# Optimization experiments

Hardware: AMD Instinct MI355X
Metric: run time of the kernel (lower is better)

The kernel has to match this reference:

```python
import jax, jax.numpy as jnp
import numpy as np

N_NODES = 50000
N_GRAPHS = 64


def _gcn_layer(x, w, b, src, dst, dinv):
    # GCNConv: out = D^{-1/2} (A+I) D^{-1/2} (x W) + b; self-loops already in src/dst
    xw = x @ w                                  # [N, out]
    norm = (dinv[src] * dinv[dst])[:, None]     # [E+N, 1]
    msgs = xw[src] * norm                       # gather + scale
    out = jax.ops.segment_sum(msgs, dst, num_segments=N_NODES)
    return out + b


def setup_inputs() -> dict:
    key = jax.random.key(0)
    ks = jax.random.split(key, 12)
    E = 800000
    F_IN, H = 128, 256
    x = jax.random.normal(ks[0], (N_NODES, F_IN), dtype=jnp.float32)
    edge_attr = jax.random.normal(ks[1], (E, 4), dtype=jnp.float32)
    edge_index = jax.random.randint(ks[2], (2, E), 0, N_NODES, dtype=jnp.int64)
    batch = jnp.sort(jax.random.randint(ks[3], (N_NODES,), 0, N_GRAPHS, dtype=jnp.int64))
    def glorot(k, fi, fo):
        s = jnp.sqrt(6.0 / (fi + fo))
        return jax.random.uniform(k, (fi, fo), minval=-s, maxval=s, dtype=jnp.float32)
    return {
        "x": x, "edge_attr": edge_attr, "edge_index": edge_index, "batch": batch,
        "w1": glorot(ks[4], F_IN, H), "b1": jnp.zeros((H,), jnp.float32),
        "w2": glorot(ks[5], H, H), "b2": jnp.zeros((H,), jnp.float32),
        "w3": glorot(ks[6], H, H), "b3": jnp.zeros((H,), jnp.float32),
        "lin1_w": glorot(ks[7], H, H // 2), "lin1_b": jnp.zeros((H // 2,), jnp.float32),
        "lin2_w": glorot(ks[8], H // 2, 3), "lin2_b": jnp.zeros((3,), jnp.float32),
    }


def reference(x, edge_attr, edge_index, batch, w1, b1, w2, b2, w3, b3,
              lin1_w, lin1_b, lin2_w, lin2_b):
    # add self-loops once; shared by all three conv layers
    loop = jnp.arange(N_NODES, dtype=edge_index.dtype)
    src = jnp.concatenate([edge_index[0], loop])
    dst = jnp.concatenate([edge_index[1], loop])
    deg = jax.ops.segment_sum(jnp.ones_like(dst, dtype=x.dtype), dst, num_segments=N_NODES)
    dinv = jnp.where(deg > 0, jax.lax.rsqrt(deg), 0.0)

    h = jax.nn.relu(_gcn_layer(x, w1, b1, src, dst, dinv))
    h = jax.nn.relu(_gcn_layer(h, w2, b2, src, dst, dinv))
    h = _gcn_layer(h, w3, b3, src, dst, dinv)

    # global mean pool over graphs
    sums = jax.ops.segment_sum(h, batch, num_segments=N_GRAPHS)
    cnts = jax.ops.segment_sum(jnp.ones((h.shape[0],), h.dtype), batch, num_segments=N_GRAPHS)
    pooled = sums / jnp.maximum(cnts, 1.0)[:, None]

    # eval mode: dropout is identity
    out = pooled @ lin1_w + lin1_b
    out = out @ lin2_w + lin2_b
    return out
```

## Files before the change

### kernel.cpp

```cpp
#include <hip/hip_runtime.h>
#include <cstdint>

constexpr int NG = 64;
constexpr int H  = 256;

typedef __bf16 bf16x8 __attribute__((ext_vector_type(8)));
typedef float  f32x4  __attribute__((ext_vector_type(4)));

__device__ __forceinline__ uint32_t pk_bf16(float a, float b) {
    uint32_t ua = __builtin_bit_cast(uint32_t, a);
    uint32_t ub = __builtin_bit_cast(uint32_t, b);
    ua += 0x7fffu + ((ua >> 16) & 1u);
    ub += 0x7fffu + ((ub >> 16) & 1u);
    return (ua >> 16) | (ub & 0xffff0000u);
}
__device__ __forceinline__ ushort bf16r(float x) {
    uint32_t u = __builtin_bit_cast(uint32_t, x);
    u += 0x7fffu + ((u >> 16) & 1u);
    return (ushort)(u >> 16);
}
__device__ __forceinline__ float bf2f(ushort h) {
    return __builtin_bit_cast(float, ((uint32_t)h) << 16);
}
__device__ __forceinline__ void bf2acc(uint32_t u, float& a0, float& a1) {
    a0 += __builtin_bit_cast(float, u << 16);
    a1 += __builtin_bit_cast(float, u & 0xffff0000u);
}

__global__ void hist_kernel(const int* __restrict__ dst, int* __restrict__ cnt, int E) {
    int e = blockIdx.x * blockDim.x + threadIdx.x;
    if (e < E) atomicAdd(&cnt[dst[e]], 1);
}

__global__ __launch_bounds__(256) void scanA(const int* __restrict__ cnt, int* __restrict__ bsum,
                                             float* __restrict__ dinv, int n) {
    __shared__ int sh[256];
    int t = threadIdx.x, i = blockIdx.x * 256 + t;
    int v = (i < n) ? cnt[i] : 0;
    if (i < n) dinv[i] = rsqrtf((float)(v + 1));
    sh[t] = v;
    __syncthreads();
    for (int off = 128; off > 0; off >>= 1) {
        if (t < off) sh[t] += sh[t + off];
        __syncthreads();
    }
    if (t == 0) bsum[blockIdx.x] = sh[0];
}

__global__ __launch_bounds__(256) void scanB(const int* __restrict__ bsum, int* __restrict__ boff,
                                             int* __restrict__ total_out, int nb) {
    __shared__ int sh[256];
    int t = threadIdx.x;
    int v = (t < nb) ? bsum[t] : 0;
    sh[t] = v;
    __syncthreads();
    for (int off = 1; off < 256; off <<= 1) {
        int a = (t >= off) ? sh[t - off] : 0;
        __syncthreads();
        sh[t] += a;
        __syncthreads();
    }
    if (t < nb) boff[t] = sh[t] - v;
    if (t == nb - 1) *total_out = sh[t];
}

__global__ __launch_bounds__(256) void scanC(const int* __restrict__ cnt, const int* __restrict__ boff,
                                             int* __restrict__ row_ptr, int* __restrict__ fill, int n) {
    __shared__ int sh[256];
    int t = threadIdx.x, i = blockIdx.x * 256 + t;
    int v = (i < n) ? cnt[i] : 0;
    sh[t] = v;
    __syncthreads();
    for (int off = 1; off < 256; off <<= 1) {
        int a = (t >= off) ? sh[t - off] : 0;
        __syncthreads();
        sh[t] += a;
        __syncthreads();
    }
    if (i < n) {
        int excl = boff[blockIdx.x] + sh[t] - v;
        row_ptr[i] = excl;
        fill[i] = excl;
    }
}

__global__ void sp_kernel(const int* __restrict__ src, const int* __restrict__ dst,
                          int* __restrict__ fill, int* __restrict__ ssrc, int E,
                          const float* __restrict__ x, const float* __restrict__ dinv,
                          ushort* __restrict__ y, int np4 ) {
    int i = blockIdx.x * blockDim.x + threadIdx.x;
    if (i < E) {
        int pos = atomicAdd(&fill[dst[i]], 1);
        ssrc[pos] = src[i];
    }
    if (i < np4) {
        int f = i * 4;
        float dv = dinv[f >> 7];
        float4 v = *reinterpret_cast<const float4*>(x + f);
        uint2 o;
        o.x = pk_bf16(v.x * dv, v.y * dv);
        o.y = pk_bf16(v.z * dv, v.w * dv);
        *reinterpret_cast<uint2*>(y + f) = o;
    }
}

__global__ void wconv_kernel(const float* __restrict__ w1, ushort* __restrict__ h1, ushort* __restrict__ l1,
                             const float* __restrict__ w2, ushort* __restrict__ h2, ushort* __restrict__ l2) {
    int idx = blockIdx.x * 256 + threadIdx.x;
    const float* w; ushort *hi, *lo; int K;
    if (idx < 128 * 256) { w = w1; hi = h1; lo = l1; K = 128; }
    else { idx -= 128 * 256; if (idx >= 256 * 256) return; w = w2; hi = h2; lo = l2; K = 256; }
    int k = idx / 256, n = idx & 255;
    float v = w[idx];
    ushort h = bf16r(v);
    float r = v - bf2f(h);
    hi[n * K + k] = h;
    lo[n * K + k] = bf16r(r);
}

template<int VEC>
__global__ __launch_bounds__(256) void agg_kernel(const ushort* __restrict__ y,
                                                  const float* __restrict__ dinv,
                                                  const int* __restrict__ row_ptr,
                                                  const int* __restrict__ ssrc,
                                                  ushort* __restrict__ zout, int n) {
    constexpr int W = VEC * 64;
    int wave = threadIdx.x >> 6;
    int lane = threadIdx.x & 63;
    int node = blockIdx.x * 4 + wave;
    if (node >= n) return;
    float acc[VEC] = {};

    auto ld4 = [&](int s) -> uint2 {
        return *reinterpret_cast<const uint2*>(y + (size_t)s * W + lane * VEC);
    };
    auto ld2 = [&](int s) -> uint32_t {
        return *reinterpret_cast<const uint32_t*>(y + (size_t)s * W + lane * VEC);
    };

    if constexpr (VEC == 4) {
        uint2 v = ld4(node);
        bf2acc(v.x, acc[0], acc[1]); bf2acc(v.y, acc[2], acc[3]);
    } else {
        bf2acc(ld2(node), acc[0], acc[1]);
    }

    int beg = row_ptr[node], end = row_ptr[node + 1];
    int e = beg;
    for (; e + 8 <= end; e += 8) {
        int s[8];
        #pragma unroll
        for (int q = 0; q < 8; ++q) s[q] = ssrc[e + q];
        if constexpr (VEC == 4) {
            uint2 v[8];
            #pragma unroll
            for (int q = 0; q < 8; ++q) v[q] = ld4(s[q]);
            #pragma unroll
            for (int q = 0; q < 8; ++q) {
                bf2acc(v[q].x, acc[0], acc[1]); bf2acc(v[q].y, acc[2], acc[3]);
            }
        } else {
            uint32_t v[8];
            #pragma unroll
            for (int q = 0; q < 8; ++q) v[q] = ld2(s[q]);
            #pragma unroll
            for (int q = 0; q < 8; ++q) bf2acc(v[q], acc[0], acc[1]);
        }
    }
    for (; e + 4 <= end; e += 4) {
        int s[4];
        #pragma unroll
        for (int q = 0; q < 4; ++q) s[q] = ssrc[e + q];
        if constexpr (VEC == 4) {
            uint2 v[4];
            #pragma unroll
            for (int q = 0; q < 4; ++q) v[q] = ld4(s[q]);
            #pragma unroll
            for (int q = 0; q < 4; ++q) {
                bf2acc(v[q].x, acc[0], acc[1]); bf2acc(v[q].y, acc[2], acc[3]);
            }
        } else {
            uint32_t v[4];
            #pragma unroll
            for (int q = 0; q < 4; ++q) v[q] = ld2(s[q]);
            #pragma unroll
            for (int q = 0; q < 4; ++q) bf2acc(v[q], acc[0], acc[1]);
        }
    }
    for (; e < end; ++e) {
        if constexpr (VEC == 4) {
            uint2 v = ld4(ssrc[e]);
            bf2acc(v.x, acc[0], acc[1]); bf2acc(v.y, acc[2], acc[3]);
        } else {
            bf2acc(ld2(ssrc[e]), acc[0], acc[1]);
        }
    }

    float dv = dinv[node];
    ushort* zp = zout + (size_t)node * W + lane * VEC;
    if constexpr (VEC == 4) {
        uint2 o;
        o.x = pk_bf16(dv * acc[0], dv * acc[1]);
        o.y = pk_bf16(dv * acc[2], dv * acc[3]);
        *reinterpret_cast<uint2*>(zp) = o;
    } else {
        *reinterpret_cast<uint32_t*>(zp) = pk_bf16(dv * acc[0], dv * acc[1]);
    }
}

template<bool RELU>
__global__ __launch_bounds__(256) void mfma_gemm(const ushort* __restrict__ A,
                                                 const ushort* __restrict__ Bhi,
                                                 const ushort* __restrict__ Blo,
                                                 const float* __restrict__ bias,
                                                 const float* __restrict__ dinv,
                                                 ushort* __restrict__ C, int M, int K) {
    constexpr int BM = 128, BN = 64, BK = 64;
    constexpr int LDK = BK + 8;
    __shared__ ushort As[BM][LDK];
    __shared__ ushort Bh[BN][LDK];
    __shared__ ushort Bl[BN][LDK];

    const int tid = threadIdx.x;
    const int w = tid >> 6;
    const int l = tid & 63;
    const int lr = l & 15;
    const int lk = (l >> 4) * 8;
    const int bm = blockIdx.x * BM;
    const int bn = blockIdx.y * BN;

    f32x4 acc[8];
    #pragma unroll
    for (int i = 0; i < 8; ++i) acc[i] = (f32x4){0.f, 0.f, 0.f, 0.f};

    for (int k0 = 0; k0 < K; k0 += BK) {
        #pragma unroll
        for (int p = 0; p < 4; ++p) {
            int g = tid + p * 256;
            int r = g >> 3;
            int c = (g & 7) << 3;
            int grow = bm + r;
            uint4 va = make_uint4(0u, 0u, 0u, 0u);
            if (grow < M) va = *reinterpret_cast<const uint4*>(A + (size_t)grow * K + k0 + c);
            *reinterpret_cast<uint4*>(&As[r][c]) = va;
        }
        #pragma unroll
        for (int p = 0; p < 2; ++p) {
            int g = tid + p * 256;
            int r = g >> 3;
            int c = (g & 7) << 3;
            *reinterpret_cast<uint4*>(&Bh[r][c]) =
                *reinterpret_cast<const uint4*>(Bhi + (size_t)(bn + r) * K + k0 + c);
            *reinterpret_cast<uint4*>(&Bl[r][c]) =
                *reinterpret_cast<const uint4*>(Blo + (size_t)(bn + r) * K + k0 + c);
        }
        __syncthreads();
        #pragma unroll
        for (int kk = 0; kk < BK; kk += 32) {
            bf16x8 bh = *reinterpret_cast<const bf16x8*>(&Bh[w * 16 + lr][kk + lk]);
            bf16x8 bl = *reinterpret_cast<const bf16x8*>(&Bl[w * 16 + lr][kk + lk]);
            #pragma unroll
            for (int r16 = 0; r16 < 8; ++r16) {
                bf16x8 a = *reinterpret_cast<const bf16x8*>(&As[r16 * 16 + lr][kk + lk]);
                acc[r16] = __builtin_amdgcn_mfma_f32_16x16x32_bf16(a, bh, acc[r16], 0, 0, 0);
                acc[r16] = __builtin_amdgcn_mfma_f32_16x16x32_bf16(a, bl, acc[r16], 0, 0, 0);
            }
        }
        __syncthreads();
    }

    int col = bn + w * 16 + lr;
    float bv = bias[col];
    #pragma unroll
    for (int r16 = 0; r16 < 8; ++r16) {
        #pragma unroll
        for (int j = 0; j < 4; ++j) {
            int row = bm + r16 * 16 + (l >> 4) * 4 + j;
            if (row < M) {
                float v = acc[r16][j] + bv;
                if (RELU) v = fmaxf(v, 0.f);
                v *= dinv[row];
                C[(size_t)row * H + col] = bf16r(v);
            }
        }
    }
}

__global__ __launch_bounds__(256) void pool_kernel(const ushort* __restrict__ z,
                                                   const int* __restrict__ batch,
                                                   float* __restrict__ sums,
                                                   int* __restrict__ gcnt, int n) {
    constexpr int NCH = 128;
    int t = threadIdx.x;
    int base = blockIdx.x * NCH;
    if (base >= n) return;
    int endn = min(base + NCH, n);
    int cur = batch[base];
    float local = 0.f;
    int cl = 0;
    for (int i = base; i < endn; ++i) {
        int g = batch[i];
        if (g != cur) {
            atomicAdd(&sums[cur * H + t], local);
            if (t == 0) atomicAdd(&gcnt[cur], cl);
            local = 0.f; cl = 0; cur = g;
        }
        local += bf2f(z[(size_t)i * H + t]);
        cl++;
    }
    atomicAdd(&sums[cur * H + t], local);
    if (t == 0) atomicAdd(&gcnt[cur], cl);
}

__global__ __launch_bounds__(256) void head_kernel(const float* __restrict__ sums,
                                                   const int* __restrict__ gcnt,
                                                   const float* __restrict__ w3, const float* __restrict__ b3,
                                                   const float* __restrict__ l1w, const float* __restrict__ l1b,
                                                   const float* __restrict__ l2w, const float* __restrict__ l2b,
                                                   float* __restrict__ out) {
    __shared__ float pooled[H];
    __shared__ float t3[H];
    __shared__ float mid[H / 2];
    int g = blockIdx.x, t = threadIdx.x;
    float c = (float)max(gcnt[g], 1);
    pooled[t] = sums[g * H + t] / c;
    __syncthreads();
    float a = b3[t];
    for (int k = 0; k < H; ++k) a += pooled[k] * w3[k * H + t];
    t3[t] = a;
    __syncthreads();
    if (t < H / 2) {
        float m = l1b[t];
        for (int k = 0; k < H; ++k) m += t3[k] * l1w[k * (H / 2) + t];
        mid[t] = m;
    }
    __syncthreads();
    if (t < 3) {
        float o = l2b[t];
        for (int k = 0; k < H / 2; ++k) o += mid[k] * l2w[k * 3 + t];
        out[g * 3 + t] = o;
    }
}

extern "C" void kernel_launch(void* const* d_in, const int* in_sizes, int n_in,
                              void* d_out, int out_size, void* d_ws, size_t ws_size,
                              hipStream_t stream) {
    const float* x   = (const float*)d_in[0];
    const int*   ei  = (const int*)d_in[2];
    const int*   bat = (const int*)d_in[3];
    const float* w1  = (const float*)d_in[4];
    const float* b1  = (const float*)d_in[5];
    const float* w2  = (const float*)d_in[6];
    const float* b2  = (const float*)d_in[7];
    const float* w3  = (const float*)d_in[8];
    const float* b3  = (const float*)d_in[9];
    const float* l1w = (const float*)d_in[10];
    const float* l1b = (const float*)d_in[11];
    const float* l2w = (const float*)d_in[12];
    const float* l2b = (const float*)d_in[13];
    float* out = (float*)d_out;

    const int N = in_sizes[0] / 128;
    const int E = in_sizes[2] / 2;
    const int NB = (N + 255) / 256;

    char* ws = (char*)d_ws;
    size_t off = 0;
    auto alloc = [&](size_t bytes) {
        void* p = ws + off;
        off = (off + bytes + 255) & ~(size_t)255;
        return p;
    };
    ushort* yb     = (ushort*)alloc((size_t)N * H * 2);
    ushort* z16    = (ushort*)alloc((size_t)N * H * 2);
    int*    cnt    = (int*)alloc((size_t)N * 4);
    float*  dinv   = (float*)alloc((size_t)N * 4);
    int*    row_ptr= (int*)alloc((size_t)(N + 1) * 4);
    int*    fill   = (int*)alloc((size_t)N * 4);
    int*    ssrc   = (int*)alloc((size_t)E * 4);
    int*    bsum   = (int*)alloc(256 * 4);
    int*    boff   = (int*)alloc(256 * 4);
    ushort* wt1h   = (ushort*)alloc((size_t)128 * 256 * 2);
    ushort* wt1l   = (ushort*)alloc((size_t)128 * 256 * 2);
    ushort* wt2h   = (ushort*)alloc((size_t)256 * 256 * 2);
    ushort* wt2l   = (ushort*)alloc((size_t)256 * 256 * 2);
    float*  sums   = (float*)alloc((size_t)NG * H * 4);
    int*    gcnt   = (int*)alloc((size_t)NG * 4);

    hipMemsetAsync(cnt, 0, (size_t)N * 4, stream);
    hipMemsetAsync(sums, 0, (size_t)NG * H * 4, stream);
    hipMemsetAsync(gcnt, 0, (size_t)NG * 4, stream);

    hist_kernel<<<(E + 255) / 256, 256, 0, stream>>>(ei + E, cnt, E);
    scanA<<<NB, 256, 0, stream>>>(cnt, bsum, dinv, N);
    scanB<<<1, 256, 0, stream>>>(bsum, boff, row_ptr + N, NB);
    scanC<<<NB, 256, 0, stream>>>(cnt, boff, row_ptr, fill, N);
    wconv_kernel<<<(128 * 256 + 256 * 256) / 256, 256, 0, stream>>>(w1, wt1h, wt1l, w2, wt2h, wt2l);
    sp_kernel<<<(N * 32 + 255) / 256, 256, 0, stream>>>(ei, ei + E, fill, ssrc, E,
                                                        x, dinv, yb, N * 32);

    agg_kernel<2><<<(N + 3) / 4, 256, 0, stream>>>(yb, dinv, row_ptr, ssrc, z16, N);
    mfma_gemm<true><<<dim3((N + 127) / 128, 4), 256, 0, stream>>>(z16, wt1h, wt1l, b1, dinv, yb, N, 128);

    agg_kernel<4><<<(N + 3) / 4, 256, 0, stream>>>(yb, dinv, row_ptr, ssrc, z16, N);
    mfma_gemm<true><<<dim3((N + 127) / 128, 4), 256, 0, stream>>>(z16, wt2h, wt2l, b2, dinv, yb, N, 256);

    agg_kernel<4><<<(N + 3) / 4, 256, 0, stream>>>(yb, dinv, row_ptr, ssrc, z16, N);

    pool_kernel<<<(N + 127) / 128, 256, 0, stream>>>(z16, bat, sums, gcnt, N);
    head_kernel<<<NG, 256, 0, stream>>>(sums, gcnt, w3, b3, l1w, l1b, l2w, l2b, out);
}
```

Baseline: 470.0 us.

## Store features in 32-column chunk planes and split aggregation per chunk

Feature matrices move from row-major to a chunked layout of [K/32][N][32] bf16, so each aggregation block gathers only 64-byte rows from one plane, which should improve cache locality. One wave now processes four edges at a time using 16-lane groups and reduces with shuffles. The source indices in the sorted edge list are stored as 16-bit values to halve that traffic, which only works while N is at most 65535. The weight-conversion and scatter kernels are merged, and the sums/count memsets move into scanB to cut launches.

```diff
diff --git a/kernel.cpp b/kernel.cpp
--- a/kernel.cpp
+++ b/kernel.cpp
@@ -48,9 +48,12 @@
 }
 
 __global__ __launch_bounds__(256) void scanB(const int* __restrict__ bsum, int* __restrict__ boff,
-                                             int* __restrict__ total_out, int nb) {
+                                             int* __restrict__ total_out, int nb,
+                                             float* __restrict__ sums, int* __restrict__ gcnt) {
     __shared__ int sh[256];
     int t = threadIdx.x;
+    for (int i = t; i < NG * H; i += 256) sums[i] = 0.f;
+    if (t < NG) gcnt[t] = 0;
     int v = (t < nb) ? bsum[t] : 0;
     sh[t] = v;
     __syncthreads();
@@ -84,127 +87,80 @@
     }
 }
 
-__global__ void sp_kernel(const int* __restrict__ src, const int* __restrict__ dst,
-                          int* __restrict__ fill, int* __restrict__ ssrc, int E,
-                          const float* __restrict__ x, const float* __restrict__ dinv,
-                          ushort* __restrict__ y, int np4 ) {
-    int i = blockIdx.x * blockDim.x + threadIdx.x;
+constexpr int WCONV_BLOCKS = (128 * 256 + 256 * 256) / 256;
+__global__ void wsp_kernel(const float* __restrict__ w1, ushort* __restrict__ h1, ushort* __restrict__ l1,
+                           const float* __restrict__ w2, ushort* __restrict__ h2, ushort* __restrict__ l2,
+                           const int* __restrict__ src, const int* __restrict__ dst,
+                           int* __restrict__ fill, ushort* __restrict__ ssrc, int E,
+                           const float* __restrict__ x, const float* __restrict__ dinv,
+                           ushort* __restrict__ y, int N) {
+    if (blockIdx.x < WCONV_BLOCKS) {
+        int idx = blockIdx.x * 256 + threadIdx.x;
+        const float* w; ushort *hi, *lo; int K;
+        if (idx < 128 * 256) { w = w1; hi = h1; lo = l1; K = 128; }
+        else { idx -= 128 * 256; w = w2; hi = h2; lo = l2; K = 256; }
+        int k = idx / 256, n = idx & 255;
+        float v = w[idx];
+        ushort h = bf16r(v);
+        float r = v - bf2f(h);
+        hi[n * K + k] = h;
+        lo[n * K + k] = bf16r(r);
+        return;
+    }
+    int i = (blockIdx.x - WCONV_BLOCKS) * 256 + threadIdx.x;
     if (i < E) {
         int pos = atomicAdd(&fill[dst[i]], 1);
-        ssrc[pos] = src[i];
-    }
+        ssrc[pos] = (ushort)src[i];
+    }
+    int np4 = N * 32;
     if (i < np4) {
         int f = i * 4;
-        float dv = dinv[f >> 7];
+        int node = f >> 7;
+        int k = f & 127;
+        float dv = dinv[node];
         float4 v = *reinterpret_cast<const float4*>(x + f);
         uint2 o;
         o.x = pk_bf16(v.x * dv, v.y * dv);
         o.y = pk_bf16(v.z * dv, v.w * dv);
-        *reinterpret_cast<uint2*>(y + f) = o;
-    }
-}
-
-__global__ void wconv_kernel(const float* __restrict__ w1, ushort* __restrict__ h1, ushort* __restrict__ l1,
-                             const float* __restrict__ w2, ushort* __restrict__ h2, ushort* __restrict__ l2) {
-    int idx = blockIdx.x * 256 + threadIdx.x;
-    const float* w; ushort *hi, *lo; int K;
-    if (idx < 128 * 256) { w = w1; hi = h1; lo = l1; K = 128; }
-    else { idx -= 128 * 256; if (idx >= 256 * 256) return; w = w2; hi = h2; lo = l2; K = 256; }
-    int k = idx / 256, n = idx & 255;
-    float v = w[idx];
-    ushort h = bf16r(v);
-    float r = v - bf2f(h);
-    hi[n * K + k] = h;
-    lo[n * K + k] = bf16r(r);
-}
-
-template<int VEC>
+        *reinterpret_cast<uint2*>(y + ((size_t)(k >> 5) * N + node) * 32 + (k & 31)) = o;
+    }
+}
+
+template<int NC>
 __global__ __launch_bounds__(256) void agg_kernel(const ushort* __restrict__ y,
                                                   const float* __restrict__ dinv,
                                                   const int* __restrict__ row_ptr,
-                                                  const int* __restrict__ ssrc,
+                                                  const ushort* __restrict__ ssrc,
                                                   ushort* __restrict__ zout, int n) {
-    constexpr int W = VEC * 64;
     int wave = threadIdx.x >> 6;
     int lane = threadIdx.x & 63;
-    int node = blockIdx.x * 4 + wave;
+    int chunk = blockIdx.x % NC;
+    int node = (blockIdx.x / NC) * 4 + wave;
     if (node >= n) return;
-    float acc[VEC] = {};
-
-    auto ld4 = [&](int s) -> uint2 {
-        return *reinterpret_cast<const uint2*>(y + (size_t)s * W + lane * VEC);
-    };
-    auto ld2 = [&](int s) -> uint32_t {
-        return *reinterpret_cast<const uint32_t*>(y + (size_t)s * W + lane * VEC);
-    };
-
-    if constexpr (VEC == 4) {
-        uint2 v = ld4(node);
-        bf2acc(v.x, acc[0], acc[1]); bf2acc(v.y, acc[2], acc[3]);
-    } else {
-        bf2acc(ld2(node), acc[0], acc[1]);
-    }
-
+    int es = lane >> 4;
+    int fd = lane & 15;
+    const size_t plane = (size_t)chunk * n;
+
+    float a0 = 0.f, a1 = 0.f;
+    if (es == 0) {
+        uint32_t u = *reinterpret_cast<const uint32_t*>(y + (plane + node) * 32 + fd * 2);
+        bf2acc(u, a0, a1);
+    }
     int beg = row_ptr[node], end = row_ptr[node + 1];
-    int e = beg;
-    for (; e + 8 <= end; e += 8) {
-        int s[8];
-        #pragma unroll
-        for (int q = 0; q < 8; ++q) s[q] = ssrc[e + q];
-        if constexpr (VEC == 4) {
-            uint2 v[8];
-            #pragma unroll
-            for (int q = 0; q < 8; ++q) v[q] = ld4(s[q]);
-            #pragma unroll
-            for (int q = 0; q < 8; ++q) {
-                bf2acc(v[q].x, acc[0], acc[1]); bf2acc(v[q].y, acc[2], acc[3]);
-            }
-        } else {
-            uint32_t v[8];
-            #pragma unroll
-            for (int q = 0; q < 8; ++q) v[q] = ld2(s[q]);
-            #pragma unroll
-            for (int q = 0; q < 8; ++q) bf2acc(v[q], acc[0], acc[1]);
-        }
-    }
-    for (; e + 4 <= end; e += 4) {
-        int s[4];
-        #pragma unroll
-        for (int q = 0; q < 4; ++q) s[q] = ssrc[e + q];
-        if constexpr (VEC == 4) {
-            uint2 v[4];
-            #pragma unroll
-            for (int q = 0; q < 4; ++q) v[q] = ld4(s[q]);
-            #pragma unroll
-            for (int q = 0; q < 4; ++q) {
-                bf2acc(v[q].x, acc[0], acc[1]); bf2acc(v[q].y, acc[2], acc[3]);
-            }
-        } else {
-            uint32_t v[4];
-            #pragma unroll
-            for (int q = 0; q < 4; ++q) v[q] = ld2(s[q]);
-            #pragma unroll
-            for (int q = 0; q < 4; ++q) bf2acc(v[q], acc[0], acc[1]);
-        }
-    }
-    for (; e < end; ++e) {
-        if constexpr (VEC == 4) {
-            uint2 v = ld4(ssrc[e]);
-            bf2acc(v.x, acc[0], acc[1]); bf2acc(v.y, acc[2], acc[3]);
-        } else {
-            bf2acc(ld2(ssrc[e]), acc[0], acc[1]);
-        }
-    }
-
-    float dv = dinv[node];
-    ushort* zp = zout + (size_t)node * W + lane * VEC;
-    if constexpr (VEC == 4) {
-        uint2 o;
-        o.x = pk_bf16(dv * acc[0], dv * acc[1]);
-        o.y = pk_bf16(dv * acc[2], dv * acc[3]);
-        *reinterpret_cast<uint2*>(zp) = o;
-    } else {
-        *reinterpret_cast<uint32_t*>(zp) = pk_bf16(dv * acc[0], dv * acc[1]);
+    for (int e = beg; e < end; e += 4) {
+        int ee = e + es;
+        uint32_t u = 0;
+        if (ee < end) {
+            int s = ssrc[ee];
+            u = *reinterpret_cast<const uint32_t*>(y + (plane + s) * 32 + fd * 2);
+        }
+        bf2acc(u, a0, a1);
+    }
+    a0 += __shfl_xor(a0, 16); a1 += __shfl_xor(a1, 16);
+    a0 += __shfl_xor(a0, 32); a1 += __shfl_xor(a1, 32);
+    if (es == 0) {
+        float dv = dinv[node];
+        *reinterpret_cast<uint32_t*>(zout + (plane + node) * 32 + fd * 2) = pk_bf16(dv * a0, dv * a1);
     }
 }
 
@@ -240,8 +196,10 @@
             int r = g >> 3;
             int c = (g & 7) << 3;
             int grow = bm + r;
+            int gk = k0 + c;
             uint4 va = make_uint4(0u, 0u, 0u, 0u);
-            if (grow < M) va = *reinterpret_cast<const uint4*>(A + (size_t)grow * K + k0 + c);
+            if (grow < M)
+                va = *reinterpret_cast<const uint4*>(A + ((size_t)(gk >> 5) * M + grow) * 32 + (gk & 31));
             *reinterpret_cast<uint4*>(&As[r][c]) = va;
         }
         #pragma unroll
@@ -270,6 +228,7 @@
     }
 
     int col = bn + w * 16 + lr;
+    int cc = col >> 5, co = col & 31;
     float bv = bias[col];
     #pragma unroll
     for (int r16 = 0; r16 < 8; ++r16) {
@@ -280,7 +239,7 @@
                 float v = acc[r16][j] + bv;
                 if (RELU) v = fmaxf(v, 0.f);
                 v *= dinv[row];
-                C[(size_t)row * H + col] = bf16r(v);
+                C[((size_t)cc * M + row) * 32 + co] = bf16r(v);
             }
         }
     }
@@ -295,6 +254,8 @@
     int base = blockIdx.x * NCH;
     if (base >= n) return;
     int endn = min(base + NCH, n);
+    size_t poff = (size_t)(t >> 5) * n;
+    int co = t & 31;
     int cur = batch[base];
     float local = 0.f;
     int cl = 0;
@@ -305,7 +266,7 @@
             if (t == 0) atomicAdd(&gcnt[cur], cl);
             local = 0.f; cl = 0; cur = g;
         }
-        local += bf2f(z[(size_t)i * H + t]);
+        local += bf2f(z[(poff + i) * 32 + co]);
         cl++;
     }
     atomicAdd(&sums[cur * H + t], local);
@@ -377,7 +338,7 @@
     float*  dinv   = (float*)alloc((size_t)N * 4);
     int*    row_ptr= (int*)alloc((size_t)(N + 1) * 4);
     int*    fill   = (int*)alloc((size_t)N * 4);
-    int*    ssrc   = (int*)alloc((size_t)E * 4);
+    ushort* ssrc   = (ushort*)alloc((size_t)E * 2);
     int*    bsum   = (int*)alloc(256 * 4);
     int*    boff   = (int*)alloc(256 * 4);
     ushort* wt1h   = (ushort*)alloc((size_t)128 * 256 * 2);
@@ -388,24 +349,23 @@
     int*    gcnt   = (int*)alloc((size_t)NG * 4);
 
     hipMemsetAsync(cnt, 0, (size_t)N * 4, stream);
-    hipMemsetAsync(sums, 0, (size_t)NG * H * 4, stream);
-    hipMemsetAsync(gcnt, 0, (size_t)NG * 4, stream);
 
     hist_kernel<<<(E + 255) / 256, 256, 0, stream>>>(ei + E, cnt, E);
     scanA<<<NB, 256, 0, stream>>>(cnt, bsum, dinv, N);
-    scanB<<<1, 256, 0, stream>>>(bsum, boff, row_ptr + N, NB);
+    scanB<<<1, 256, 0, stream>>>(bsum, boff, row_ptr + N, NB, sums, gcnt);
     scanC<<<NB, 256, 0, stream>>>(cnt, boff, row_ptr, fill, N);
-    wconv_kernel<<<(128 * 256 + 256 * 256) / 256, 256, 0, stream>>>(w1, wt1h, wt1l, w2, wt2h, wt2l);
-    sp_kernel<<<(N * 32 + 255) / 256, 256, 0, stream>>>(ei, ei + E, fill, ssrc, E,
-                                                        x, dinv, yb, N * 32);
-
-    agg_kernel<2><<<(N + 3) / 4, 256, 0, stream>>>(yb, dinv, row_ptr, ssrc, z16, N);
+    int sp_blocks = (N * 32 + 255) / 256;
+    wsp_kernel<<<WCONV_BLOCKS + sp_blocks, 256, 0, stream>>>(
+        w1, wt1h, wt1l, w2, wt2h, wt2l,
+        ei, ei + E, fill, ssrc, E, x, dinv, yb, N);
+
+    agg_kernel<4><<<((N + 3) / 4) * 4, 256, 0, stream>>>(yb, dinv, row_ptr, ssrc, z16, N);
     mfma_gemm<true><<<dim3((N + 127) / 128, 4), 256, 0, stream>>>(z16, wt1h, wt1l, b1, dinv, yb, N, 128);
 
-    agg_kernel<4><<<(N + 3) / 4, 256, 0, stream>>>(yb, dinv, row_ptr, ssrc, z16, N);
+    agg_kernel<8><<<((N + 3) / 4) * 8, 256, 0, stream>>>(yb, dinv, row_ptr, ssrc, z16, N);
     mfma_gemm<true><<<dim3((N + 127) / 128, 4), 256, 0, stream>>>(z16, wt2h, wt2l, b2, dinv, yb, N, 256);
 
-    agg_kernel<4><<<(N + 3) / 4, 256, 0, stream>>>(yb, dinv, row_ptr, ssrc, z16, N);
+    agg_kernel<8><<<((N + 3) / 4) * 8, 256, 0, stream>>>(yb, dinv, row_ptr, ssrc, z16, N);
 
     pool_kernel<<<(N + 127) / 128, 256, 0, stream>>>(z16, bat, sums, gcnt, N);
     head_kernel<<<NG, 256, 0, stream>>>(sums, gcnt, w3, b3, l1w, l1b, l2w, l2b, out);
```

After: 709.4 us. 50.9% more time.
